# Kernel tuning notes

Measured on AMD Instinct MI355X. Metric: run time of the kernel, lower is better.

## Reference

```python
import jax, jax.numpy as jnp
import numpy as np
from jax.scipy.special import digamma

B, D, H, K = 8192, 1024, 1024, 100
EPS_LN = 1e-5
EPS_B = 1e-8


def setup_inputs() -> dict:
    key = jax.random.key(0)
    ks = jax.random.split(key, 9)
    s = 0.02
    return {
        "x": jax.random.normal(ks[0], (B, D), jnp.float32),
        "W1": jax.random.normal(ks[1], (D, H), jnp.float32) * s,
        "b1": jnp.zeros((H,), jnp.float32),
        "g": jnp.ones((H,), jnp.float32),
        "beta": jnp.zeros((H,), jnp.float32),
        "W2": jax.random.normal(ks[2], (H, H), jnp.float32) * s,
        "b2": jnp.zeros((H,), jnp.float32),
        "W3": jax.random.normal(ks[3], (H, K), jnp.float32) * s,
        "b3": jnp.zeros((K,), jnp.float32),
    }


def _layernorm(h, g, beta):
    mu = h.mean(-1, keepdims=True)
    var = ((h - mu) ** 2).mean(-1, keepdims=True)
    return (h - mu) * jax.lax.rsqrt(var + EPS_LN) * g + beta


def reference(x, W1, b1, g, beta, W2, b2, W3, b3):
    # MLP: Linear -> SiLU -> LayerNorm -> Linear -> SiLU -> Linear
    h = jax.nn.silu(x @ W1 + b1)
    h = _layernorm(h, g, beta)
    h = jax.nn.silu(h @ W2 + b2)
    logits = h @ W3 + b3                      # (B, K)

    evidence = jax.nn.softplus(logits)
    alpha = evidence + 1.0
    S = alpha.sum(-1, keepdims=True)          # (B, 1)
    expected_prob = alpha / S
    vacuity = float(K) / S[:, 0]
    belief = evidence / S                     # (B, K)

    # dissonance: sum_{i<j} (1 - |bi-bj|/(bi+bj+eps)) * bi * bj
    # vectorized via full symmetric pairwise sum; diagonal term is b_i^2
    bi = belief[:, :, None]
    bj = belief[:, None, :]
    full = ((1.0 - jnp.abs(bi - bj) / (bi + bj + EPS_B)) * bi * bj).sum((-1, -2))
    dissonance = 0.5 * (full - (belief * belief).sum(-1))

    aleatoric = -(alpha / S * (digamma(alpha) - digamma(S))).sum(-1)
    return (alpha, evidence, expected_prob, vacuity, dissonance, aleatoric)
```

## Files before the change

### kernel.cpp

```cpp
#include <hip/hip_runtime.h>
#include <hip/hip_bf16.h>
#include <math.h>


typedef __attribute__((ext_vector_type(8))) _Float16 f16x8;
typedef __attribute__((ext_vector_type(4))) float f32x4;

__device__ __forceinline__ unsigned short f2h(float v) {
  _Float16 h = (_Float16)v;
  return *(unsigned short*)&h;
}

__device__ __forceinline__ void gld_lds16(const void* g, void* l) {
  __builtin_amdgcn_global_load_lds((const __attribute__((address_space(1))) void*)g,
                                   (__attribute__((address_space(3))) void*)l, 16, 0, 0);
}

__device__ __forceinline__ float wred64(float v) {
#pragma unroll
  for (int m = 32; m >= 1; m >>= 1) v += __shfl_xor(v, m);
  return v;
}

__device__ __forceinline__ float digammaf_(float x) {
  float r = 0.f;
  if (x < 8.f) {
    r -= __builtin_amdgcn_rcpf(x);
    r -= __builtin_amdgcn_rcpf(x + 1.f);
    r -= __builtin_amdgcn_rcpf(x + 2.f);
    r -= __builtin_amdgcn_rcpf(x + 3.f);
    r -= __builtin_amdgcn_rcpf(x + 4.f);
    r -= __builtin_amdgcn_rcpf(x + 5.f);
    r -= __builtin_amdgcn_rcpf(x + 6.f);
    x += 7.f;
  }
  float inv = __builtin_amdgcn_rcpf(x), inv2 = inv * inv;
  float s = logf(x) - 0.5f * inv
          - inv2 * (0.083333333333f - inv2 * (0.008333333333f - inv2 * 0.003968253968f));
  return r + s;
}


__global__ __launch_bounds__(256) void prep_kernel(
    const float* __restrict__ W1, const float* __restrict__ W2,
    const float* __restrict__ W3, const float* __restrict__ x,
    unsigned short* __restrict__ W1T, unsigned short* __restrict__ W2T,
    unsigned short* __restrict__ W3T, unsigned short* __restrict__ Xp) {
  __shared__ float t[32][33];
  const int b = blockIdx.x;
  const int tid = threadIdx.x;
  if (b < 2176) {
    const float* W; unsigned short* Th; int Ncols, idx;
    if (b < 1024)      { W = W1; Th = W1T; Ncols = 1024; idx = b; }
    else if (b < 2048) { W = W2; Th = W2T; Ncols = 1024; idx = b - 1024; }
    else               { W = W3; Th = W3T; Ncols = 100;  idx = b - 2048; }
    int k0 = (idx & 31) * 32, n0 = (idx >> 5) * 32;
#pragma unroll
    for (int i = 0; i < 4; ++i) {
      int e = i * 256 + tid;
      int r = e >> 5, c = e & 31;
      int gn = n0 + c;
      t[r][c] = (gn < Ncols) ? W[(size_t)(k0 + r) * Ncols + gn] : 0.f;
    }
    __syncthreads();
    int nr = tid >> 3, t2 = tid & 7;
    ushort4 h;
    h.x = f2h(t[t2 * 4 + 0][nr]); h.y = f2h(t[t2 * 4 + 1][nr]);
    h.z = f2h(t[t2 * 4 + 2][nr]); h.w = f2h(t[t2 * 4 + 3][nr]);
    int n = n0 + nr;
    int q = t2 >> 1, half = t2 & 1;
    int qs = q ^ ((n >> 1) & 3);
    size_t base = ((size_t)(n >> 7) * 32 + (k0 >> 5)) * 4096
                + (n & 127) * 32 + (qs << 3) + (half << 2);
    *(ushort4*)(Th + base) = h;
  } else {
    int idx = (b - 2176) * 256 + tid;
    int r = idx >> 7;
    int k0 = (idx & 127) * 8;
    const float* sp = x + (size_t)r * 1024 + k0;
    const float4 v0 = *(const float4*)sp;
    const float4 v1 = *(const float4*)(sp + 4);
    ushort4 h0, h1;
    h0.x = f2h(v0.x); h0.y = f2h(v0.y); h0.z = f2h(v0.z); h0.w = f2h(v0.w);
    h1.x = f2h(v1.x); h1.y = f2h(v1.y); h1.z = f2h(v1.z); h1.w = f2h(v1.w);
    int q = (k0 & 31) >> 3;
    int qs = q ^ ((r >> 1) & 3);
    size_t base = ((size_t)(r >> 7) * 32 + (k0 >> 5)) * 4096
                + (r & 127) * 32 + (qs << 3);
    *(ushort4*)(Xp + base) = h0; *(ushort4*)(Xp + base + 4) = h1;
  }
}

template <int MODE>
__global__ __launch_bounds__(512, 4) void gemm_f16(
    const unsigned short* __restrict__ Ap, const unsigned short* __restrict__ Bp,
    const float* __restrict__ bias, float* __restrict__ C,
    unsigned short* __restrict__ Op) {
  constexpr int NT = (MODE == 1) ? 4 : 32;
  __shared__ __align__(16) unsigned short lds[16384];
  const int tid = threadIdx.x;
  const int lane = tid & 63;
  const int wave = tid >> 6;
  const int wm = wave >> 1;
  const int wn = wave & 1;
  const int row0 = blockIdx.x * 128;
  const int col0 = blockIdx.y * 128;
  const int kbase = (MODE == 1) ? blockIdx.z * 4 : 0;
  const int lsrc = lane * 8;
  const size_t abase = (size_t)blockIdx.x * 32 * 4096;
  const size_t bbase = (size_t)blockIdx.y * 32 * 4096;

  f32x4 acc[2][4] = {};

  auto STAGE = [&](int bb, int t) {
    const size_t ac = abase + (size_t)(kbase + t) * 4096;
    const size_t bc = bbase + (size_t)(kbase + t) * 4096;
    const int lb = bb * 8192;
    const int so = wave * 512;
    gld_lds16(Ap + ac + so + lsrc, &lds[lb + so]);
    gld_lds16(Bp + bc + so + lsrc, &lds[lb + 4096 + so]);
  };

  STAGE(0, 0);
  for (int t = 0; t < NT; ++t) {
    __syncthreads();
    if (t + 1 < NT) STAGE((t + 1) & 1, t + 1);
    const int lb = (t & 1) * 8192;
    const int cc = lane >> 4;
    f16x8 ah[2], bh[4];
#pragma unroll
    for (int a = 0; a < 2; ++a) {
      int r = wm * 32 + a * 16 + (lane & 15);
      int off = lb + r * 32 + ((cc ^ ((r >> 1) & 3)) << 3);
      ah[a] = *(const f16x8*)&lds[off];
    }
#pragma unroll
    for (int b = 0; b < 4; ++b) {
      int n = wn * 64 + b * 16 + (lane & 15);
      int off = lb + 4096 + n * 32 + ((cc ^ ((n >> 1) & 3)) << 3);
      bh[b] = *(const f16x8*)&lds[off];
    }
#pragma unroll
    for (int a = 0; a < 2; ++a)
#pragma unroll
      for (int b = 0; b < 4; ++b)
        acc[a][b] = __builtin_amdgcn_mfma_f32_16x16x32_f16(ah[a], bh[b], acc[a][b], 0, 0, 0);
  }
#pragma unroll
  for (int a = 0; a < 2; ++a) {
    int rb = row0 + wm * 32 + a * 16 + (lane >> 4) * 4;
#pragma unroll
    for (int b = 0; b < 4; ++b) {
      int col = col0 + wn * 64 + b * 16 + (lane & 15);
      if (MODE == 0) {
        float bi = bias[col];
#pragma unroll
        for (int j = 0; j < 4; ++j) {
          float v = acc[a][b][j] + bi;
          v = v / (1.f + expf(-v));
          C[(size_t)(rb + j) * 1024 + col] = v;
        }
      } else if (MODE == 1) {
        if (col < 100) {
          float* Cz = C + (size_t)blockIdx.z * 819200;
#pragma unroll
          for (int j = 0; j < 4; ++j)
            Cz[(size_t)(rb + j) * 100 + col] = acc[a][b][j];
        }
      } else {
        float bi = bias[col];
        int q = (col & 31) >> 3, p = col & 7;
        size_t cb = ((size_t)blockIdx.x * 32 + (col >> 5)) * 4096 + p;
#pragma unroll
        for (int j = 0; j < 4; ++j) {
          float v = acc[a][b][j] + bi;
          v = v / (1.f + expf(-v));
          int rr = rb + j;
          size_t base = cb + (size_t)(rr & 127) * 32 + ((q ^ ((rr >> 1) & 3)) << 3);
          Op[base] = f2h(v);
        }
      }
    }
  }
}

__global__ __launch_bounds__(256) void ln_kernel(
    const float* __restrict__ Hin, const float* __restrict__ gw,
    const float* __restrict__ bw, unsigned short* __restrict__ Op) {
  __shared__ float sb[8];
  int row = blockIdx.x, tid = threadIdx.x;
  const float4 v = ((const float4*)(Hin + (size_t)row * 1024))[tid];
  float s1 = v.x + v.y + v.z + v.w;
  float s2 = v.x * v.x + v.y * v.y + v.z * v.z + v.w * v.w;
  s1 = wred64(s1); s2 = wred64(s2);
  if ((tid & 63) == 0) { sb[tid >> 6] = s1; sb[4 + (tid >> 6)] = s2; }
  __syncthreads();
  s1 = sb[0] + sb[1] + sb[2] + sb[3];
  s2 = sb[4] + sb[5] + sb[6] + sb[7];
  float mu = s1 * 0.0009765625f;
  float var = s2 * 0.0009765625f - mu * mu;
  float inv = rsqrtf(var + 1e-5f);
  const float4 gv = ((const float4*)gw)[tid];
  const float4 bv = ((const float4*)bw)[tid];
  ushort4 h;
  h.x = f2h((v.x - mu) * inv * gv.x + bv.x);
  h.y = f2h((v.y - mu) * inv * gv.y + bv.y);
  h.z = f2h((v.z - mu) * inv * gv.z + bv.z);
  h.w = f2h((v.w - mu) * inv * gv.w + bv.w);
  int k = tid * 4;
  int q = (k & 31) >> 3, half = (k >> 2) & 1;
  int qs = q ^ ((row >> 1) & 3);
  size_t base = ((size_t)(row >> 7) * 32 + (k >> 5)) * 4096
              + (row & 127) * 32 + (qs << 3) + (half << 2);
  *(ushort4*)(Op + base) = h;
}

__global__ __launch_bounds__(256) void head_kernel(
    const float* __restrict__ part, const float* __restrict__ b3,
    float* __restrict__ out) {
  __shared__ float bel[4][184];
  int tid = threadIdx.x;
  int wave = tid >> 6, lane = tid & 63;
  int row = blockIdx.x * 4 + wave;
  size_t rb = (size_t)row * 100;
  bool v1 = lane < 36;
  float l0 = b3[lane];
  float l1 = v1 ? b3[lane + 64] : 0.f;
#pragma unroll
  for (int z = 0; z < 8; ++z) {
    const float* pz = part + (size_t)z * 819200 + rb;
    l0 += pz[lane];
    if (v1) l1 += pz[lane + 64];
  }
  float e0 = fmaxf(l0, 0.f) + log1pf(expf(-fabsf(l0)));
  float e1 = fmaxf(l1, 0.f) + log1pf(expf(-fabsf(l1)));
  float a0 = e0 + 1.f, a1 = e1 + 1.f;
  float S = 100.f + wred64(e0 + (v1 ? e1 : 0.f));
  float invS = 1.f / S;
  float b0 = e0 * invS;
  float b1 = v1 ? e1 * invS : 0.f;
  bel[wave][lane] = b0;
  if (v1) bel[wave][lane + 64] = b1;
  bel[wave][lane + 100] = (lane < 50) ? b0 : 0.f;
  if (lane < 16) bel[wave][lane + 164] = 0.f;
  __syncthreads();
  const float* bp = &bel[wave][0];
  float b0e = b0 + 1e-8f;
  float b1e = b1 + 1e-8f;
  float acc = 0.f;
#pragma unroll
  for (int d = 1; d <= 50; ++d) {
    float bj0 = bp[lane + d];
    float bj1 = bp[lane + 64 + d];
    float p0 = b0 * bj0;
    float p1 = b1 * bj1;
    float q0 = p0 * fabsf(b0 - bj0);
    float q1 = p1 * fabsf(b1 - bj1);
    float r0 = __builtin_amdgcn_rcpf(b0e + bj0);
    float r1 = __builtin_amdgcn_rcpf(b1e + bj1);
    float t = (p0 - q0 * r0) + (p1 - q1 * r1);
    acc += (d == 50) ? 0.5f * t : t;
  }
  float diss = wred64(acc);
  float dgS = digammaf_(S);
  float t0 = a0 * invS * (digammaf_(a0) - dgS);
  float t1 = v1 ? a1 * invS * (digammaf_(a1) - dgS) : 0.f;
  float ale = -wred64(t0 + t1);
  out[rb + lane] = a0;
  out[819200 + rb + lane] = e0;
  out[1638400 + rb + lane] = a0 * invS;
  if (v1) {
    out[rb + lane + 64] = a1;
    out[819200 + rb + lane + 64] = e1;
    out[1638400 + rb + lane + 64] = a1 * invS;
  }
  if (lane == 0) {
    out[2457600 + row] = 100.f * invS;
    out[2457600 + 8192 + row] = diss;
    out[2457600 + 16384 + row] = ale;
  }
}

extern "C" void kernel_launch(void* const* d_in, const int* in_sizes, int n_in,
                              void* d_out, int out_size, void* d_ws, size_t ws_size,
                              hipStream_t stream) {
  const float* x  = (const float*)d_in[0];
  const float* W1 = (const float*)d_in[1];
  const float* b1 = (const float*)d_in[2];
  const float* g  = (const float*)d_in[3];
  const float* be = (const float*)d_in[4];
  const float* W2 = (const float*)d_in[5];
  const float* b2 = (const float*)d_in[6];
  const float* W3 = (const float*)d_in[7];
  const float* b3 = (const float*)d_in[8];
  float* out = (float*)d_out;

  char* w = (char*)d_ws;
  unsigned short* R0p  = (unsigned short*)(w);
  unsigned short* W1T  = (unsigned short*)(w + (32ll << 20));
  unsigned short* W2T  = (unsigned short*)(w + (34ll << 20));
  unsigned short* W3T  = (unsigned short*)(w + (36ll << 20));
  float*          hF   = (float*)(w + (41ll << 20));
  unsigned short* H2p  = (unsigned short*)(w + (41ll << 20));
  float*          parts = (float*)(w);

  dim3 blk(256);
  dim3 blk512(512);
  hipLaunchKernelGGL(prep_kernel, dim3(6272), blk, 0, stream,
                     W1, W2, W3, x, W1T, W2T, W3T, R0p);
  hipLaunchKernelGGL((gemm_f16<0>), dim3(64, 8), blk512, 0, stream,
                     R0p, W1T, b1, hF, (unsigned short*)nullptr);
  hipLaunchKernelGGL(ln_kernel, dim3(8192), blk, 0, stream, hF, g, be, R0p);
  hipLaunchKernelGGL((gemm_f16<2>), dim3(64, 8), blk512, 0, stream,
                     R0p, W2T, b2, (float*)nullptr, H2p);
  hipLaunchKernelGGL((gemm_f16<1>), dim3(64, 1, 8), blk512, 0, stream,
                     H2p, W3T, b3, parts, (unsigned short*)nullptr);
  hipLaunchKernelGGL(head_kernel, dim3(2048), blk, 0, stream, parts, b3, out);
  (void)in_sizes; (void)n_in; (void)out_size; (void)ws_size;
}
```

Measured before the change: 187.7 us.

## Fold LayerNorm into second GEMM via gamma-scaled weights and atomic row stats

Removes the standalone LayerNorm kernel and the fp32 hidden write/read. The first GEMM now writes SiLU output directly as packed fp16 and atomically accumulates per-row sum and sum of squares. The second GEMM applies the normalization algebraically: W2 is prescaled by gamma, and the epilogue uses inv*acc - mu*inv*u + (b2 + beta·W2). Risks come from precision loss in the unnormalized fp16 activations, E[x^2]-mu^2 cancellation, atomic contention, and a serial 1024-iteration column-reduction in the prep kernel.

New measurement: 226.3 us. 20.6% more time.

```diff
diff --git a/kernel.cpp b/kernel.cpp
--- a/kernel.cpp
+++ b/kernel.cpp
@@ -44,16 +44,20 @@
 __global__ __launch_bounds__(256) void prep_kernel(
     const float* __restrict__ W1, const float* __restrict__ W2,
     const float* __restrict__ W3, const float* __restrict__ x,
+    const float* __restrict__ gw, const float* __restrict__ be,
+    const float* __restrict__ b2,
     unsigned short* __restrict__ W1T, unsigned short* __restrict__ W2T,
-    unsigned short* __restrict__ W3T, unsigned short* __restrict__ Xp) {
+    unsigned short* __restrict__ W3T, unsigned short* __restrict__ Xp,
+    float* __restrict__ ub, float* __restrict__ bias2,
+    float* __restrict__ stats) {
   __shared__ float t[32][33];
   const int b = blockIdx.x;
   const int tid = threadIdx.x;
   if (b < 2176) {
-    const float* W; unsigned short* Th; int Ncols, idx;
-    if (b < 1024)      { W = W1; Th = W1T; Ncols = 1024; idx = b; }
-    else if (b < 2048) { W = W2; Th = W2T; Ncols = 1024; idx = b - 1024; }
-    else               { W = W3; Th = W3T; Ncols = 100;  idx = b - 2048; }
+    const float* W; unsigned short* Th; int Ncols, idx; bool scale;
+    if (b < 1024)      { W = W1; Th = W1T; Ncols = 1024; idx = b; scale = false; }
+    else if (b < 2048) { W = W2; Th = W2T; Ncols = 1024; idx = b - 1024; scale = true; }
+    else               { W = W3; Th = W3T; Ncols = 100;  idx = b - 2048; scale = false; }
     int k0 = (idx & 31) * 32, n0 = (idx >> 5) * 32;
 #pragma unroll
     for (int i = 0; i < 4; ++i) {
@@ -64,16 +68,21 @@
     }
     __syncthreads();
     int nr = tid >> 3, t2 = tid & 7;
+    int kk = k0 + t2 * 4;
+    float v0 = t[t2 * 4 + 0][nr], v1 = t[t2 * 4 + 1][nr];
+    float v2 = t[t2 * 4 + 2][nr], v3 = t[t2 * 4 + 3][nr];
+    if (scale) {
+      v0 *= gw[kk + 0]; v1 *= gw[kk + 1]; v2 *= gw[kk + 2]; v3 *= gw[kk + 3];
+    }
     ushort4 h;
-    h.x = f2h(t[t2 * 4 + 0][nr]); h.y = f2h(t[t2 * 4 + 1][nr]);
-    h.z = f2h(t[t2 * 4 + 2][nr]); h.w = f2h(t[t2 * 4 + 3][nr]);
+    h.x = f2h(v0); h.y = f2h(v1); h.z = f2h(v2); h.w = f2h(v3);
     int n = n0 + nr;
     int q = t2 >> 1, half = t2 & 1;
     int qs = q ^ ((n >> 1) & 3);
     size_t base = ((size_t)(n >> 7) * 32 + (k0 >> 5)) * 4096
                 + (n & 127) * 32 + (qs << 3) + (half << 2);
     *(ushort4*)(Th + base) = h;
-  } else {
+  } else if (b < 6272) {
     int idx = (b - 2176) * 256 + tid;
     int r = idx >> 7;
     int k0 = (idx & 127) * 8;
@@ -88,6 +97,19 @@
     size_t base = ((size_t)(r >> 7) * 32 + (k0 >> 5)) * 4096
                 + (r & 127) * 32 + (qs << 3);
     *(ushort4*)(Xp + base) = h0; *(ushort4*)(Xp + base + 4) = h1;
+  } else if (b < 6276) {
+    int n = (b - 6272) * 256 + tid;
+    float uu = 0.f, vb = 0.f;
+    for (int k = 0; k < 1024; ++k) {
+      float w = W2[(size_t)k * 1024 + n];
+      uu += gw[k] * w;
+      vb += be[k] * w;
+    }
+    ub[n] = uu;
+    bias2[n] = b2[n] + vb;
+  } else {
+    int idx = (b - 6276) * 256 + tid;
+    ((float4*)stats)[idx] = float4{0.f, 0.f, 0.f, 0.f};
   }
 }
 
@@ -95,7 +117,8 @@
 __global__ __launch_bounds__(512, 4) void gemm_f16(
     const unsigned short* __restrict__ Ap, const unsigned short* __restrict__ Bp,
     const float* __restrict__ bias, float* __restrict__ C,
-    unsigned short* __restrict__ Op) {
+    unsigned short* __restrict__ Op, const float* __restrict__ u,
+    float* __restrict__ stats) {
   constexpr int NT = (MODE == 1) ? 4 : 32;
   __shared__ __align__(16) unsigned short lds[16384];
   const int tid = threadIdx.x;
@@ -146,73 +169,65 @@
       for (int b = 0; b < 4; ++b)
         acc[a][b] = __builtin_amdgcn_mfma_f32_16x16x32_f16(ah[a], bh[b], acc[a][b], 0, 0, 0);
   }
-#pragma unroll
-  for (int a = 0; a < 2; ++a) {
-    int rb = row0 + wm * 32 + a * 16 + (lane >> 4) * 4;
-#pragma unroll
-    for (int b = 0; b < 4; ++b) {
-      int col = col0 + wn * 64 + b * 16 + (lane & 15);
-      if (MODE == 0) {
-        float bi = bias[col];
-#pragma unroll
-        for (int j = 0; j < 4; ++j) {
-          float v = acc[a][b][j] + bi;
-          v = v / (1.f + expf(-v));
-          C[(size_t)(rb + j) * 1024 + col] = v;
-        }
-      } else if (MODE == 1) {
+  if (MODE == 1) {
+#pragma unroll
+    for (int a = 0; a < 2; ++a) {
+      int rb = row0 + wm * 32 + a * 16 + (lane >> 4) * 4;
+#pragma unroll
+      for (int b = 0; b < 4; ++b) {
+        int col = col0 + wn * 64 + b * 16 + (lane & 15);
         if (col < 100) {
           float* Cz = C + (size_t)blockIdx.z * 819200;
 #pragma unroll
           for (int j = 0; j < 4; ++j)
             Cz[(size_t)(rb + j) * 100 + col] = acc[a][b][j];
         }
-      } else {
-        float bi = bias[col];
-        int q = (col & 31) >> 3, p = col & 7;
-        size_t cb = ((size_t)blockIdx.x * 32 + (col >> 5)) * 4096 + p;
-#pragma unroll
-        for (int j = 0; j < 4; ++j) {
-          float v = acc[a][b][j] + bi;
+      }
+    }
+  } else {
+#pragma unroll
+    for (int a = 0; a < 2; ++a) {
+      int rb = row0 + wm * 32 + a * 16 + (lane >> 4) * 4;
+#pragma unroll
+      for (int j = 0; j < 4; ++j) {
+        int rr = rb + j;
+        float inv = 0.f, cS = 0.f;
+        if (MODE == 4) {
+          float s1 = stats[(rr << 1) + 0], s2 = stats[(rr << 1) + 1];
+          float mu = s1 * 0.0009765625f;
+          float var = s2 * 0.0009765625f - mu * mu;
+          inv = rsqrtf(var + 1e-5f);
+          cS = -mu * inv;
+        }
+        float vs = 0.f, vq = 0.f;
+        const size_t rbase = (size_t)blockIdx.x * 32 * 4096 + (size_t)(rr & 127) * 32;
+        const int rsw = (rr >> 1) & 3;
+#pragma unroll
+        for (int b = 0; b < 4; ++b) {
+          int col = col0 + wn * 64 + b * 16 + (lane & 15);
+          float v;
+          if (MODE == 4) v = inv * acc[a][b][j] + cS * u[col] + bias[col];
+          else           v = acc[a][b][j] + bias[col];
           v = v / (1.f + expf(-v));
-          int rr = rb + j;
-          size_t base = cb + (size_t)(rr & 127) * 32 + ((q ^ ((rr >> 1) & 3)) << 3);
+          int q = (col & 31) >> 3, p = col & 7;
+          size_t base = rbase + (size_t)(col >> 5) * 4096 + ((q ^ rsw) << 3) + p;
           Op[base] = f2h(v);
+          if (MODE == 3) { vs += v; vq += v * v; }
+        }
+        if (MODE == 3) {
+#pragma unroll
+          for (int m = 1; m <= 8; m <<= 1) {
+            vs += __shfl_xor(vs, m);
+            vq += __shfl_xor(vq, m);
+          }
+          if ((lane & 15) == 0) {
+            atomicAdd(&stats[(rr << 1) + 0], vs);
+            atomicAdd(&stats[(rr << 1) + 1], vq);
+          }
         }
       }
     }
   }
-}
-
-__global__ __launch_bounds__(256) void ln_kernel(
-    const float* __restrict__ Hin, const float* __restrict__ gw,
-    const float* __restrict__ bw, unsigned short* __restrict__ Op) {
-  __shared__ float sb[8];
-  int row = blockIdx.x, tid = threadIdx.x;
-  const float4 v = ((const float4*)(Hin + (size_t)row * 1024))[tid];
-  float s1 = v.x + v.y + v.z + v.w;
-  float s2 = v.x * v.x + v.y * v.y + v.z * v.z + v.w * v.w;
-  s1 = wred64(s1); s2 = wred64(s2);
-  if ((tid & 63) == 0) { sb[tid >> 6] = s1; sb[4 + (tid >> 6)] = s2; }
-  __syncthreads();
-  s1 = sb[0] + sb[1] + sb[2] + sb[3];
-  s2 = sb[4] + sb[5] + sb[6] + sb[7];
-  float mu = s1 * 0.0009765625f;
-  float var = s2 * 0.0009765625f - mu * mu;
-  float inv = rsqrtf(var + 1e-5f);
-  const float4 gv = ((const float4*)gw)[tid];
-  const float4 bv = ((const float4*)bw)[tid];
-  ushort4 h;
-  h.x = f2h((v.x - mu) * inv * gv.x + bv.x);
-  h.y = f2h((v.y - mu) * inv * gv.y + bv.y);
-  h.z = f2h((v.z - mu) * inv * gv.z + bv.z);
-  h.w = f2h((v.w - mu) * inv * gv.w + bv.w);
-  int k = tid * 4;
-  int q = (k & 31) >> 3, half = (k >> 2) & 1;
-  int qs = q ^ ((row >> 1) & 3);
-  size_t base = ((size_t)(row >> 7) * 32 + (k >> 5)) * 4096
-              + (row & 127) * 32 + (qs << 3) + (half << 2);
-  *(ushort4*)(Op + base) = h;
 }
 
 __global__ __launch_bounds__(256) void head_kernel(
@@ -296,25 +311,28 @@
   float* out = (float*)d_out;
 
   char* w = (char*)d_ws;
-  unsigned short* R0p  = (unsigned short*)(w);
-  unsigned short* W1T  = (unsigned short*)(w + (32ll << 20));
-  unsigned short* W2T  = (unsigned short*)(w + (34ll << 20));
-  unsigned short* W3T  = (unsigned short*)(w + (36ll << 20));
-  float*          hF   = (float*)(w + (41ll << 20));
-  unsigned short* H2p  = (unsigned short*)(w + (41ll << 20));
+  unsigned short* Xp    = (unsigned short*)(w);
+  unsigned short* W1T   = (unsigned short*)(w + (32ll << 20));
+  unsigned short* W2T   = (unsigned short*)(w + (34ll << 20));
+  unsigned short* W3T   = (unsigned short*)(w + (36ll << 20));
+  float*          stats = (float*)(w + (37ll << 20));
+  float*          ub    = (float*)(w + (37ll << 20) + (64ll << 10));
+  float*          bias2 = (float*)(w + (37ll << 20) + (68ll << 10));
+  unsigned short* H1p   = (unsigned short*)(w + (41ll << 20));
+  unsigned short* H2p   = (unsigned short*)(w + (57ll << 20));
   float*          parts = (float*)(w);
 
   dim3 blk(256);
   dim3 blk512(512);
-  hipLaunchKernelGGL(prep_kernel, dim3(6272), blk, 0, stream,
-                     W1, W2, W3, x, W1T, W2T, W3T, R0p);
-  hipLaunchKernelGGL((gemm_f16<0>), dim3(64, 8), blk512, 0, stream,
-                     R0p, W1T, b1, hF, (unsigned short*)nullptr);
-  hipLaunchKernelGGL(ln_kernel, dim3(8192), blk, 0, stream, hF, g, be, R0p);
-  hipLaunchKernelGGL((gemm_f16<2>), dim3(64, 8), blk512, 0, stream,
-                     R0p, W2T, b2, (float*)nullptr, H2p);
+  hipLaunchKernelGGL(prep_kernel, dim3(6292), blk, 0, stream,
+                     W1, W2, W3, x, g, be, b2, W1T, W2T, W3T, Xp, ub, bias2, stats);
+  hipLaunchKernelGGL((gemm_f16<3>), dim3(64, 8), blk512, 0, stream,
+                     Xp, W1T, b1, (float*)nullptr, H1p, (const float*)nullptr, stats);
+  hipLaunchKernelGGL((gemm_f16<4>), dim3(64, 8), blk512, 0, stream,
+                     H1p, W2T, bias2, (float*)nullptr, H2p, ub, stats);
   hipLaunchKernelGGL((gemm_f16<1>), dim3(64, 1, 8), blk512, 0, stream,
-                     H2p, W3T, b3, parts, (unsigned short*)nullptr);
+                     H2p, W3T, (const float*)nullptr, parts, (unsigned short*)nullptr,
+                     (const float*)nullptr, (float*)nullptr);
   hipLaunchKernelGGL(head_kernel, dim3(2048), blk, 0, stream, parts, b3, out);
   (void)in_sizes; (void)n_in; (void)out_size; (void)ws_size;
 }
```
